# Kernel tuning notes

Measured on AMD Instinct MI355X. Metric: run time of the kernel, lower is better.

## Reference

```python
import jax, jax.numpy as jnp
import numpy as np

B, C, L, E = 65536, 16, 32, 32
EPS = 1e-12

def _normalize(x, axis=-1):
    # F.normalize: x / max(||x||_2, eps)
    n = jnp.sqrt(jnp.sum(x * x, axis=axis, keepdims=True))
    return x / jnp.maximum(n, EPS)

def _linear(x, W, b):
    # torch nn.Linear: y = x @ W.T + b, W: [out, in]
    return jnp.einsum('bcl,el->bce', x, W) + b

def setup_inputs() -> dict:
    key = jax.random.key(0)
    ks = jax.random.split(key, 12)
    s_l = 1.0 / np.sqrt(L)
    s_p1 = 1.0 / np.sqrt(C * E)
    s_p2 = 1.0 / np.sqrt(C * 3)
    return {
        'embed1': jax.random.normal(ks[0], (B, C, L), jnp.float32),
        'embed2': jax.random.normal(ks[1], (B, C, L), jnp.float32),
        'qW': jax.random.uniform(ks[2], (E, L), jnp.float32, -s_l, s_l),
        'qb': jax.random.uniform(ks[3], (E,), jnp.float32, -s_l, s_l),
        'kW': jax.random.uniform(ks[4], (E, L), jnp.float32, -s_l, s_l),
        'kb': jax.random.uniform(ks[5], (E,), jnp.float32, -s_l, s_l),
        'vW': jax.random.uniform(ks[6], (E, L), jnp.float32, -s_l, s_l),
        'vb': jax.random.uniform(ks[7], (E,), jnp.float32, -s_l, s_l),
        'p1W': jax.random.uniform(ks[8], (C * 3, C * E), jnp.float32, -s_p1, s_p1),
        'p1b': jax.random.uniform(ks[9], (C * 3,), jnp.float32, -s_p1, s_p1),
        'p2W': jax.random.uniform(ks[10], (3, C * 3), jnp.float32, -s_p2, s_p2),
        'p2b': jax.random.uniform(ks[11], (3,), jnp.float32, -s_p2, s_p2),
    }

def reference(embed1, embed2, qW, qb, kW, kb, vW, vb, p1W, p1b, p2W, p2b):
    query = _linear(embed1, qW, qb) * _linear(embed2, qW, qb)   # [B,C,E]
    key_t = _linear(embed1, kW, kb) * _linear(embed2, kW, kb)   # [B,C,E]
    value = _linear(embed1, vW, vb) * _linear(embed2, vW, vb)   # [B,C,E]
    attn = jnp.einsum('bce,bde->bcd', _normalize(query), _normalize(key_t))  # [B,C,C]
    # torch F.softmax with dim=None on a 3-D tensor -> legacy dim=0 (batch axis)
    attn = jax.nn.softmax(attn, axis=0)
    # dropout(p=0.2) is identity in eval mode
    out = jnp.einsum('bcd,bce->bde', attn, value)  # attn.transpose(1,2) @ value, [B,C,E]
    h = out.reshape(out.shape[0], -1)              # [B, C*E]
    h = jax.nn.relu(h @ p1W.T + p1b) @ p2W.T + p2b  # [B, 3]
    return _normalize(h)
```

## Files before the change

kernel.cpp:

```cpp
#include <hip/hip_runtime.h>

#define B_TOT 65536
#define WS_P1W 4096
#define WS_EV  (1u << 20)
#define EV_BYTES 100663296u
#define WS_PART (WS_EV + EV_BYTES)

typedef float f32x4 __attribute__((ext_vector_type(4)));
typedef short s16x8 __attribute__((ext_vector_type(8)));

__device__ __forceinline__ float bf2f(unsigned short h) {
    unsigned u = ((unsigned)h) << 16;
    return __builtin_bit_cast(float, u);
}
__device__ __forceinline__ unsigned pack2(float a, float b) {
    unsigned ua = __builtin_bit_cast(unsigned, a) + 0x8000u;
    unsigned ub = __builtin_bit_cast(unsigned, b) + 0x8000u;
    return __builtin_amdgcn_perm(ub, ua, 0x07060302u);
}
__device__ __forceinline__ unsigned short f2bf(float f) {
    return (unsigned short)((__builtin_bit_cast(unsigned, f) + 0x8000u) >> 16);
}
__device__ __forceinline__ s16x8 cvt8(float4 a, float4 b) {
    uint4 u;
    u.x = pack2(a.x, a.y); u.y = pack2(a.z, a.w);
    u.z = pack2(b.x, b.y); u.w = pack2(b.z, b.w);
    return __builtin_bit_cast(s16x8, u);
}
#define MFMA(a, b, c) __builtin_amdgcn_mfma_f32_16x16x32_bf16((a), (b), (c), 0, 0, 0)

__global__ __launch_bounds__(256) void k1_stats(
    const float* __restrict__ e1, const float* __restrict__ e2,
    const float* __restrict__ qW, const float* __restrict__ qb,
    const float* __restrict__ kW, const float* __restrict__ kb,
    const float* __restrict__ vW, const float* __restrict__ vb,
    char* __restrict__ ws) {

    const int tid = threadIdx.x;
    const int lane = tid & 63;
    const int widx = tid >> 6;
    const int col = lane & 15;
    const int quad = lane >> 4;

    __shared__ __align__(16) unsigned short qk_lds[4][2][16 * 40];
    __shared__ float Dblk[256];
    Dblk[tid] = 0.f;
    __syncthreads();

    s16x8 wq[2], wk[2], wv[2];
    float bq[2], bk[2], bv[2];
#pragma unroll
    for (int h = 0; h < 2; ++h) {
        int row = col + 16 * h;
        const float4* pq = (const float4*)(qW + row * 32 + quad * 8);
        const float4* pk = (const float4*)(kW + row * 32 + quad * 8);
        const float4* pv = (const float4*)(vW + row * 32 + quad * 8);
        wq[h] = cvt8(pq[0], pq[1]);
        wk[h] = cvt8(pk[0], pk[1]);
        wv[h] = cvt8(pv[0], pv[1]);
        bq[h] = qb[row]; bk[h] = kb[row]; bv[h] = vb[row];
    }

    unsigned short* qbuf = qk_lds[widx][0];
    unsigned short* kbuf = qk_lds[widx][1];
    float dacc[4] = {0.f, 0.f, 0.f, 0.f};
    char* evbase = ws + WS_EV;
    const f32x4 z = {0.f, 0.f, 0.f, 0.f};

    const int gw = blockIdx.x * 4 + widx;
    const float* p1base = e1 + (size_t)gw * 8 * 512 + col * 32 + quad * 8;
    const float* p2base = e2 + (size_t)gw * 8 * 512 + col * 32 + quad * 8;

    float4 na0 = *(const float4*)(p1base);
    float4 na1 = *(const float4*)(p1base + 4);
    float4 nb0 = *(const float4*)(p2base);
    float4 nb1 = *(const float4*)(p2base + 4);

    for (int i = 0; i < 8; ++i) {
        const int b = gw * 8 + i;
        float4 a0 = na0, a1 = na1, b0 = nb0, b1 = nb1;
        if (i < 7) {
            const float* q1p = p1base + (i + 1) * 512;
            const float* q2p = p2base + (i + 1) * 512;
            na0 = *(const float4*)(q1p);
            na1 = *(const float4*)(q1p + 4);
            nb0 = *(const float4*)(q2p);
            nb1 = *(const float4*)(q2p + 4);
        }
        s16x8 fx1 = cvt8(a0, a1);
        s16x8 fx2 = cvt8(b0, b1);

        f32x4 q1v[2], q2v[2], k1v[2], k2v[2], v1v[2], v2v[2];
#pragma unroll
        for (int h = 0; h < 2; ++h) {
            q1v[h] = MFMA(fx1, wq[h], z); q2v[h] = MFMA(fx2, wq[h], z);
            k1v[h] = MFMA(fx1, wk[h], z); k2v[h] = MFMA(fx2, wk[h], z);
            v1v[h] = MFMA(fx1, wv[h], z); v2v[h] = MFMA(fx2, wv[h], z);
        }
        float Qt[2][4], Kt[2][4], Vv[2][4];
#pragma unroll
        for (int h = 0; h < 2; ++h)
#pragma unroll
            for (int r = 0; r < 4; ++r) {
                Qt[h][r] = (q1v[h][r] + bq[h]) * (q2v[h][r] + bq[h]);
                Kt[h][r] = (k1v[h][r] + bk[h]) * (k2v[h][r] + bk[h]);
                Vv[h][r] = (v1v[h][r] + bv[h]) * (v2v[h][r] + bv[h]);
            }
#pragma unroll
        for (int r = 0; r < 4; ++r) {
            int w = (quad * 4 + r) * 20 + col;
            ((unsigned*)qbuf)[w] = pack2(Qt[0][r], Qt[1][r]);
            ((unsigned*)kbuf)[w] = pack2(Kt[0][r], Kt[1][r]);
        }
        s16x8 aq = *(const s16x8*)(qbuf + col * 40 + quad * 8);
        s16x8 bk8 = *(const s16x8*)(kbuf + col * 40 + quad * 8);
        float qv[8], kv[8], ssq = 0.f, ssk = 0.f;
#pragma unroll
        for (int j = 0; j < 8; ++j) {
            qv[j] = bf2f((unsigned short)aq[j]); ssq += qv[j] * qv[j];
            kv[j] = bf2f((unsigned short)bk8[j]); ssk += kv[j] * kv[j];
        }
        ssq += __shfl_xor(ssq, 16); ssq += __shfl_xor(ssq, 32);
        ssk += __shfl_xor(ssk, 16); ssk += __shfl_xor(ssk, 32);
        float sq = 1.f / fmaxf(sqrtf(ssq), 1e-12f);
        float sk = 1.f / fmaxf(sqrtf(ssk), 1e-12f);
        uint4 uq, uk;
        uq.x = pack2(qv[0] * sq, qv[1] * sq); uq.y = pack2(qv[2] * sq, qv[3] * sq);
        uq.z = pack2(qv[4] * sq, qv[5] * sq); uq.w = pack2(qv[6] * sq, qv[7] * sq);
        uk.x = pack2(kv[0] * sk, kv[1] * sk); uk.y = pack2(kv[2] * sk, kv[3] * sk);
        uk.z = pack2(kv[4] * sk, kv[5] * sk); uk.w = pack2(kv[6] * sk, kv[7] * sk);
        aq = __builtin_bit_cast(s16x8, uq);
        bk8 = __builtin_bit_cast(s16x8, uk);
        f32x4 S = MFMA(aq, bk8, z);

        char* bbase = evbase + (size_t)b * 1536;
        float ex[4];
#pragma unroll
        for (int r = 0; r < 4; ++r) { ex[r] = __expf(S[r]); dacc[r] += ex[r]; }
        uint2 est; est.x = pack2(ex[0], ex[1]); est.y = pack2(ex[2], ex[3]);
        *(uint2*)(bbase + col * 32 + quad * 8) = est;
#pragma unroll
        for (int h = 0; h < 2; ++h) {
            uint2 vst;
            vst.x = pack2(Vv[h][0], Vv[h][1]);
            vst.y = pack2(Vv[h][2], Vv[h][3]);
            *(uint2*)(bbase + 512 + ((h * 16 + col) * 2 + (quad >> 1)) * 16 + (quad & 1) * 8) = vst;
        }
    }
#pragma unroll
    for (int r = 0; r < 4; ++r)
        atomicAdd(&Dblk[col * 16 + quad * 4 + r], dacc[r]);
    __syncthreads();
    ((float*)(ws + WS_PART))[blockIdx.x * 256 + tid] = Dblk[tid];
}

__global__ __launch_bounds__(256) void k1b_prep(const float* __restrict__ p1W,
                                                char* __restrict__ ws) {
    const int t = threadIdx.x;
    const int idx = blockIdx.x * 256 + t;
    if (idx < 24576) {
        int jj   = idx & 7;
        int lane = (idx >> 3) & 63;
        int ktnt = idx >> 9;
        int kt = ktnt & 15, nt = ktnt >> 4;
        int n_lo = lane & 15, q8 = lane >> 4;
        int j2  = nt * 16 + n_lo;
        int ip  = kt * 32 + q8 * 8 + jj;
        int e_lo = ip >> 5, qq = (ip >> 3) & 3, hh = (ip >> 2) & 1, r = ip & 3;
        int orig = (qq * 4 + r) * 32 + (e_lo + 16 * hh);
        ((unsigned short*)(ws + WS_P1W))[idx] = f2bf(p1W[j2 * 512 + orig]);
    }
    const float* part = (const float*)(ws + WS_PART);
    const int j = blockIdx.x;
    float s = 0.f;
#pragma unroll
    for (int k = 0; k < 8; ++k)
        s += part[(size_t)(k * 256 + t) * 256 + j];
    __shared__ float red[256];
    red[t] = s;
    __syncthreads();
    for (int o = 128; o > 0; o >>= 1) {
        if (t < o) red[t] += red[t + o];
        __syncthreads();
    }
    if (t == 0) ((float*)ws)[j] = 1.f / red[0];
}

__global__ __launch_bounds__(256) void k2_apply(
    const char* __restrict__ ws, const float* __restrict__ p1b,
    const float* __restrict__ p2W, const float* __restrict__ p2b,
    float* __restrict__ out) {

    const int tid = threadIdx.x;
    const int lane = tid & 63;
    const int widx = tid >> 6;
    const int col = lane & 15;
    const int quad = lane >> 4;
    const int qm = quad & 1;

    __shared__ __align__(16) unsigned short Hs[16 * 512];
    float* P = (float*)Hs;

    float p1bias[3], p2w[3][3];
#pragma unroll
    for (int nt = 0; nt < 3; ++nt) {
        p1bias[nt] = p1b[col + 16 * nt];
#pragma unroll
        for (int t2 = 0; t2 < 3; ++t2) p2w[nt][t2] = p2W[t2 * 48 + col + 16 * nt];
    }
    const float pb0 = p2b[0], pb1 = p2b[1], pb2 = p2b[2];

    const float* Dws = (const float*)ws;
    const float4 dva = *(const float4*)(Dws + col * 16 + qm * 8);
    const float4 dvb = *(const float4*)(Dws + col * 16 + qm * 8 + 4);
    float dinv[8] = {dva.x, dva.y, dva.z, dva.w, dvb.x, dvb.y, dvb.z, dvb.w};

    const char* evbase = ws + WS_EV;
    const unsigned short* p1wp = (const unsigned short*)(ws + WS_P1W);
    const int g = blockIdx.x;
    const f32x4 z = {0.f, 0.f, 0.f, 0.f};
    const s16x8 zz = {0, 0, 0, 0, 0, 0, 0, 0};

    {
        const char* bb0 = evbase + (size_t)(g * 16 + widx * 4) * 1536;
        const int eoff  = col * 32 + qm * 16;
        const int voff0 = 512 + (col * 2 + qm) * 16;
        const int voff1 = 512 + ((16 + col) * 2 + qm) * 16;
        s16x8 ne  = *(const s16x8*)(bb0 + eoff);
        s16x8 nv0 = *(const s16x8*)(bb0 + voff0);
        s16x8 nv1 = *(const s16x8*)(bb0 + voff1);
#pragma unroll
        for (int ii = 0; ii < 4; ++ii) {
            s16x8 eraw = ne, bf0 = nv0, bf1 = nv1;
            if (ii < 3) {
                const char* nb = bb0 + (size_t)(ii + 1) * 1536;
                ne  = *(const s16x8*)(nb + eoff);
                nv0 = *(const s16x8*)(nb + voff0);
                nv1 = *(const s16x8*)(nb + voff1);
            }
            float ef[8];
#pragma unroll
            for (int j = 0; j < 8; ++j)
                ef[j] = bf2f((unsigned short)eraw[j]) * dinv[j];
            uint4 ua;
            ua.x = pack2(ef[0], ef[1]); ua.y = pack2(ef[2], ef[3]);
            ua.z = pack2(ef[4], ef[5]); ua.w = pack2(ef[6], ef[7]);
            s16x8 afrag = __builtin_bit_cast(s16x8, ua);
            if (quad >= 2) { afrag = zz; bf0 = zz; bf1 = zz; }
            f32x4 o0 = MFMA(afrag, bf0, z);
            f32x4 o1 = MFMA(afrag, bf1, z);
            uint4 uh;
            uh.x = pack2(o0[0], o0[1]); uh.y = pack2(o0[2], o0[3]);
            uh.z = pack2(o1[0], o1[1]); uh.w = pack2(o1[2], o1[3]);
            const int i = widx * 4 + ii;
            int chunk = (col * 4 + quad) ^ (i & 7);
            *(uint4*)(Hs + i * 512 + chunk * 8) = uh;
        }
    }
    __syncthreads();

    f32x4 acc[3] = {z, z, z};
    {
        const int kt0 = widx * 4;
        s16x8 nw0 = *(const s16x8*)(p1wp + ((0 * 16 + kt0) * 64 + lane) * 8);
        s16x8 nw1 = *(const s16x8*)(p1wp + ((1 * 16 + kt0) * 64 + lane) * 8);
        s16x8 nw2 = *(const s16x8*)(p1wp + ((2 * 16 + kt0) * 64 + lane) * 8);
#pragma unroll
        for (int t2 = 0; t2 < 4; ++t2) {
            const int kt = widx * 4 + t2;
            s16x8 w0 = nw0, w1 = nw1, w2 = nw2;
            if (t2 < 3) {
                nw0 = *(const s16x8*)(p1wp + ((0 * 16 + kt + 1) * 64 + lane) * 8);
                nw1 = *(const s16x8*)(p1wp + ((1 * 16 + kt + 1) * 64 + lane) * 8);
                nw2 = *(const s16x8*)(p1wp + ((2 * 16 + kt + 1) * 64 + lane) * 8);
            }
            int chunk = (kt * 4 + quad) ^ (col & 7);
            s16x8 a = *(const s16x8*)(Hs + col * 512 + chunk * 8);
            acc[0] = MFMA(a, w0, acc[0]);
            acc[1] = MFMA(a, w1, acc[1]);
            acc[2] = MFMA(a, w2, acc[2]);
        }
    }
    __syncthreads();

#pragma unroll
    for (int nt = 0; nt < 3; ++nt)
        *(f32x4*)(P + (widx * 64 + lane) * 12 + nt * 4) = acc[nt];
    __syncthreads();

    {
        float s3[3] = {0.f, 0.f, 0.f};
#pragma unroll
        for (int w = 0; w < 4; ++w)
#pragma unroll
            for (int nt = 0; nt < 3; ++nt)
                s3[nt] += P[(w * 64 + lane) * 12 + nt * 4 + widx];
        float pp[3] = {0.f, 0.f, 0.f};
#pragma unroll
        for (int nt = 0; nt < 3; ++nt) {
            float hv = fmaxf(s3[nt] + p1bias[nt], 0.f);
            pp[0] += hv * p2w[nt][0];
            pp[1] += hv * p2w[nt][1];
            pp[2] += hv * p2w[nt][2];
        }
#pragma unroll
        for (int m = 1; m <= 8; m <<= 1) {
            pp[0] += __shfl_xor(pp[0], m);
            pp[1] += __shfl_xor(pp[1], m);
            pp[2] += __shfl_xor(pp[2], m);
        }
        float h0 = pp[0] + pb0, h1 = pp[1] + pb1, h2 = pp[2] + pb2;
        float inv = 1.f / fmaxf(sqrtf(h0 * h0 + h1 * h1 + h2 * h2), 1e-12f);
        if (col < 3) {
            float v = (col == 0) ? h0 : ((col == 1) ? h1 : h2);
            out[(size_t)(g * 16 + quad * 4 + widx) * 3 + col] = v * inv;
        }
    }
}

extern "C" void kernel_launch(void* const* d_in, const int* in_sizes, int n_in,
                              void* d_out, int out_size, void* d_ws, size_t ws_size,
                              hipStream_t stream) {
    const float* e1  = (const float*)d_in[0];
    const float* e2  = (const float*)d_in[1];
    const float* qW  = (const float*)d_in[2];
    const float* qb  = (const float*)d_in[3];
    const float* kW  = (const float*)d_in[4];
    const float* kb  = (const float*)d_in[5];
    const float* vW  = (const float*)d_in[6];
    const float* vb  = (const float*)d_in[7];
    const float* p1W = (const float*)d_in[8];
    const float* p1b = (const float*)d_in[9];
    const float* p2W = (const float*)d_in[10];
    const float* p2b = (const float*)d_in[11];
    float* out = (float*)d_out;
    char* ws = (char*)d_ws;

    k1_stats<<<2048, 256, 0, stream>>>(e1, e2, qW, qb, kW, kb, vW, vb, ws);
    k1b_prep<<<256, 256, 0, stream>>>(p1W, ws);
    k2_apply<<<4096, 256, 0, stream>>>(ws, p1b, p2W, p2b, out);
}
```

Before: 341.4 us.

## Fold biases into MFMA accumulators and apply normalization after the QK product

Biases are broadcast into the MFMA accumulator inputs, so the separate bias adds go away. The Q/K/V projections are split into scoped blocks to shorten register live ranges. Normalization is no longer applied to Q and K before the score MFMA; the raw bf16 product is scaled afterwards by the shuffled inverse norms, which removes a repack. Manual prefetching of the next batch's inputs is dropped in favour of direct loads, which may expose load latency. Rounding changes slightly because unnormalized values go through the MFMA.

```diff
diff --git a/kernel.cpp b/kernel.cpp
--- a/kernel.cpp
+++ b/kernel.cpp
@@ -48,7 +48,7 @@
     __syncthreads();
 
     s16x8 wq[2], wk[2], wv[2];
-    float bq[2], bk[2], bv[2];
+    f32x4 cbq[2], cbk[2], cbv[2];
 #pragma unroll
     for (int h = 0; h < 2; ++h) {
         int row = col + 16 * h;
@@ -58,7 +58,10 @@
         wq[h] = cvt8(pq[0], pq[1]);
         wk[h] = cvt8(pk[0], pk[1]);
         wv[h] = cvt8(pv[0], pv[1]);
-        bq[h] = qb[row]; bk[h] = kb[row]; bv[h] = vb[row];
+        float qv_ = qb[row], kv_ = kb[row], vv_ = vb[row];
+        cbq[h] = (f32x4){qv_, qv_, qv_, qv_};
+        cbk[h] = (f32x4){kv_, kv_, kv_, kv_};
+        cbv[h] = (f32x4){vv_, vv_, vv_, vv_};
     }
 
     unsigned short* qbuf = qk_lds[widx][0];
@@ -68,84 +71,86 @@
     const f32x4 z = {0.f, 0.f, 0.f, 0.f};
 
     const int gw = blockIdx.x * 4 + widx;
-    const float* p1base = e1 + (size_t)gw * 8 * 512 + col * 32 + quad * 8;
-    const float* p2base = e2 + (size_t)gw * 8 * 512 + col * 32 + quad * 8;
-
-    float4 na0 = *(const float4*)(p1base);
-    float4 na1 = *(const float4*)(p1base + 4);
-    float4 nb0 = *(const float4*)(p2base);
-    float4 nb1 = *(const float4*)(p2base + 4);
-
     for (int i = 0; i < 8; ++i) {
         const int b = gw * 8 + i;
-        float4 a0 = na0, a1 = na1, b0 = nb0, b1 = nb1;
-        if (i < 7) {
-            const float* q1p = p1base + (i + 1) * 512;
-            const float* q2p = p2base + (i + 1) * 512;
-            na0 = *(const float4*)(q1p);
-            na1 = *(const float4*)(q1p + 4);
-            nb0 = *(const float4*)(q2p);
-            nb1 = *(const float4*)(q2p + 4);
-        }
+        const float4* x1p = (const float4*)(e1 + (size_t)b * 512 + col * 32 + quad * 8);
+        const float4* x2p = (const float4*)(e2 + (size_t)b * 512 + col * 32 + quad * 8);
+        float4 a0 = x1p[0], a1 = x1p[1];
+        float4 b0 = x2p[0], b1 = x2p[1];
         s16x8 fx1 = cvt8(a0, a1);
         s16x8 fx2 = cvt8(b0, b1);
 
-        f32x4 q1v[2], q2v[2], k1v[2], k2v[2], v1v[2], v2v[2];
-#pragma unroll
-        for (int h = 0; h < 2; ++h) {
-            q1v[h] = MFMA(fx1, wq[h], z); q2v[h] = MFMA(fx2, wq[h], z);
-            k1v[h] = MFMA(fx1, wk[h], z); k2v[h] = MFMA(fx2, wk[h], z);
-            v1v[h] = MFMA(fx1, wv[h], z); v2v[h] = MFMA(fx2, wv[h], z);
-        }
-        float Qt[2][4], Kt[2][4], Vv[2][4];
-#pragma unroll
-        for (int h = 0; h < 2; ++h)
+        {
+            f32x4 q1v[2], q2v[2];
+#pragma unroll
+            for (int h = 0; h < 2; ++h) {
+                q1v[h] = MFMA(fx1, wq[h], cbq[h]);
+                q2v[h] = MFMA(fx2, wq[h], cbq[h]);
+            }
 #pragma unroll
             for (int r = 0; r < 4; ++r) {
-                Qt[h][r] = (q1v[h][r] + bq[h]) * (q2v[h][r] + bq[h]);
-                Kt[h][r] = (k1v[h][r] + bk[h]) * (k2v[h][r] + bk[h]);
-                Vv[h][r] = (v1v[h][r] + bv[h]) * (v2v[h][r] + bv[h]);
-            }
-#pragma unroll
-        for (int r = 0; r < 4; ++r) {
-            int w = (quad * 4 + r) * 20 + col;
-            ((unsigned*)qbuf)[w] = pack2(Qt[0][r], Qt[1][r]);
-            ((unsigned*)kbuf)[w] = pack2(Kt[0][r], Kt[1][r]);
-        }
-        s16x8 aq = *(const s16x8*)(qbuf + col * 40 + quad * 8);
+                int w = (quad * 4 + r) * 20 + col;
+                ((unsigned*)qbuf)[w] = pack2(q1v[0][r] * q2v[0][r],
+                                             q1v[1][r] * q2v[1][r]);
+            }
+        }
+        {
+            f32x4 k1v[2], k2v[2];
+#pragma unroll
+            for (int h = 0; h < 2; ++h) {
+                k1v[h] = MFMA(fx1, wk[h], cbk[h]);
+                k2v[h] = MFMA(fx2, wk[h], cbk[h]);
+            }
+#pragma unroll
+            for (int r = 0; r < 4; ++r) {
+                int w = (quad * 4 + r) * 20 + col;
+                ((unsigned*)kbuf)[w] = pack2(k1v[0][r] * k2v[0][r],
+                                             k1v[1][r] * k2v[1][r]);
+            }
+        }
+        char* bbase = evbase + (size_t)b * 1536;
+        {
+            f32x4 v1v[2], v2v[2];
+#pragma unroll
+            for (int h = 0; h < 2; ++h) {
+                v1v[h] = MFMA(fx1, wv[h], cbv[h]);
+                v2v[h] = MFMA(fx2, wv[h], cbv[h]);
+            }
+#pragma unroll
+            for (int h = 0; h < 2; ++h) {
+                uint2 vst;
+                vst.x = pack2(v1v[h][0] * v2v[h][0], v1v[h][1] * v2v[h][1]);
+                vst.y = pack2(v1v[h][2] * v2v[h][2], v1v[h][3] * v2v[h][3]);
+                *(uint2*)(bbase + 512 + ((h * 16 + col) * 2 + (quad >> 1)) * 16 + (quad & 1) * 8) = vst;
+            }
+        }
+
+        s16x8 aq  = *(const s16x8*)(qbuf + col * 40 + quad * 8);
         s16x8 bk8 = *(const s16x8*)(kbuf + col * 40 + quad * 8);
-        float qv[8], kv[8], ssq = 0.f, ssk = 0.f;
+        f32x4 S = MFMA(aq, bk8, z);
+
+        float ssq = 0.f, ssk = 0.f;
 #pragma unroll
         for (int j = 0; j < 8; ++j) {
-            qv[j] = bf2f((unsigned short)aq[j]); ssq += qv[j] * qv[j];
-            kv[j] = bf2f((unsigned short)bk8[j]); ssk += kv[j] * kv[j];
+            float qf = bf2f((unsigned short)aq[j]);  ssq += qf * qf;
+            float kf = bf2f((unsigned short)bk8[j]); ssk += kf * kf;
         }
         ssq += __shfl_xor(ssq, 16); ssq += __shfl_xor(ssq, 32);
         ssk += __shfl_xor(ssk, 16); ssk += __shfl_xor(ssk, 32);
-        float sq = 1.f / fmaxf(sqrtf(ssq), 1e-12f);
-        float sk = 1.f / fmaxf(sqrtf(ssk), 1e-12f);
-        uint4 uq, uk;
-        uq.x = pack2(qv[0] * sq, qv[1] * sq); uq.y = pack2(qv[2] * sq, qv[3] * sq);
-        uq.z = pack2(qv[4] * sq, qv[5] * sq); uq.w = pack2(qv[6] * sq, qv[7] * sq);
-        uk.x = pack2(kv[0] * sk, kv[1] * sk); uk.y = pack2(kv[2] * sk, kv[3] * sk);
-        uk.z = pack2(kv[4] * sk, kv[5] * sk); uk.w = pack2(kv[6] * sk, kv[7] * sk);
-        aq = __builtin_bit_cast(s16x8, uq);
-        bk8 = __builtin_bit_cast(s16x8, uk);
-        f32x4 S = MFMA(aq, bk8, z);
-
-        char* bbase = evbase + (size_t)b * 1536;
-        float ex[4];
-#pragma unroll
-        for (int r = 0; r < 4; ++r) { ex[r] = __expf(S[r]); dacc[r] += ex[r]; }
-        uint2 est; est.x = pack2(ex[0], ex[1]); est.y = pack2(ex[2], ex[3]);
+        float invq = 1.f / fmaxf(sqrtf(ssq), 1e-12f);
+        float invk = 1.f / fmaxf(sqrtf(ssk), 1e-12f);
+        float iq0 = __shfl(invq, quad * 4 + 0);
+        float iq1 = __shfl(invq, quad * 4 + 1);
+        float iq2 = __shfl(invq, quad * 4 + 2);
+        float iq3 = __shfl(invq, quad * 4 + 3);
+
+        float ex0 = __expf(S[0] * (iq0 * invk));
+        float ex1 = __expf(S[1] * (iq1 * invk));
+        float ex2 = __expf(S[2] * (iq2 * invk));
+        float ex3 = __expf(S[3] * (iq3 * invk));
+        dacc[0] += ex0; dacc[1] += ex1; dacc[2] += ex2; dacc[3] += ex3;
+        uint2 est; est.x = pack2(ex0, ex1); est.y = pack2(ex2, ex3);
         *(uint2*)(bbase + col * 32 + quad * 8) = est;
-#pragma unroll
-        for (int h = 0; h < 2; ++h) {
-            uint2 vst;
-            vst.x = pack2(Vv[h][0], Vv[h][1]);
-            vst.y = pack2(Vv[h][2], Vv[h][3]);
-            *(uint2*)(bbase + 512 + ((h * 16 + col) * 2 + (quad >> 1)) * 16 + (quad & 1) * 8) = vst;
-        }
     }
 #pragma unroll
     for (int r = 0; r < 4; ++r)
```

Measured after the change: 337.0 us. Within noise of the previous version (-1.3%).
